# Kernel tuning notes

Hardware: AMD Instinct MI355X
Metric: run time of the kernel (lower is better)

The kernel has to match this reference:

```python
import jax, jax.numpy as jnp
import numpy as np

# Problem sizes: batch B, n variables, m constraints (dense nnz pattern)
B, N, M = 256, 128, 192
# OSQP ADMM parameters (scaling=0, fixed rho; OSQP defaults)
RHO = 0.1      # step size
SIGMA = 1e-6   # regularization
ALPHA = 1.6    # relaxation
N_ITERS = 400  # fixed iteration count (jit-friendly surrogate for max_iter/tolerances)


def setup_inputs() -> dict:
    key = jax.random.key(0)
    k1, k2, k3, k4, k5, k6 = jax.random.split(key, 6)
    G = jax.random.normal(k1, (B, N, N), dtype=jnp.float32)
    # PSD quadratic cost: P = G G^T / n + 0.5 I
    P_val = jnp.einsum('bij,bkj->bik', G, G) / N + 0.5 * jnp.eye(N, dtype=jnp.float32)
    q_val = jax.random.normal(k2, (B, N), dtype=jnp.float32)
    A_val = jax.random.normal(k3, (B, M, N), dtype=jnp.float32) / jnp.sqrt(jnp.float32(N))
    # Bounds bracketing a feasible point x0 so every QP is solvable
    x0 = jax.random.normal(k4, (B, N), dtype=jnp.float32)
    z0 = jnp.einsum('bmn,bn->bm', A_val, x0)
    l_val = z0 - jnp.abs(jax.random.normal(k5, (B, M), dtype=jnp.float32)) - 0.1
    u_val = z0 + jnp.abs(jax.random.normal(k6, (B, M), dtype=jnp.float32)) + 0.1
    return {'P_val': P_val, 'q_val': q_val, 'A_val': A_val,
            'l_val': l_val, 'u_val': u_val}


def _osqp_admm(P, q, A, l, u):
    """Batched OSQP ADMM with fixed rho: solves argmin 1/2 x'Px + q'x s.t. l<=Ax<=u."""
    dt = P.dtype
    I_n = jnp.eye(N, dtype=dt)
    I_m = jnp.eye(M, dtype=dt)
    AT = jnp.swapaxes(A, -1, -2)  # [B, n, m]
    # KKT matrix [[P + sigma*I, A'], [A, -I/rho]]  -> [B, n+m, n+m]
    top = jnp.concatenate([P + SIGMA * I_n, AT], axis=-1)
    bot = jnp.concatenate([A, jnp.broadcast_to(-(1.0 / RHO) * I_m, (P.shape[0], M, M))], axis=-1)
    K = jnp.concatenate([top, bot], axis=-2)
    Kinv = jnp.linalg.inv(K)  # factorize once (rho fixed)

    x0 = jnp.zeros_like(q)
    z0 = jnp.zeros_like(l)
    y0 = jnp.zeros_like(l)

    def step(carry, _):
        x, z, y = carry
        rhs = jnp.concatenate([SIGMA * x - q, z - y / RHO], axis=-1)  # [B, n+m]
        sol = jnp.einsum('bij,bj->bi', Kinv, rhs)
        xt, nu = sol[:, :N], sol[:, N:]
        zt = z + (nu - y) / RHO
        x_new = ALPHA * xt + (1.0 - ALPHA) * x
        zc = ALPHA * zt + (1.0 - ALPHA) * z
        z_new = jnp.clip(zc + y / RHO, l, u)  # projection onto [l, u]
        y_new = y + RHO * (zc - z_new)
        return (x_new, z_new, y_new), None

    (x, z, y), _ = jax.lax.scan(step, (x0, z0, y0), None, length=N_ITERS)
    return x


def reference(P_val, q_val, A_val, l_val, u_val):
    # Returns the batch of primal solutions x_hat, shape [B, n]
    return _osqp_admm(P_val, q_val, A_val, l_val, u_val)
```

## Files before the change

### kernel.cpp

```cpp
#include <hip/hip_runtime.h>


#define Nn 128
#define Mm 192
constexpr float RHO_    = 0.1f;
constexpr float SIGMA_  = 1e-6f;
constexpr float ALPHA_  = 1.6f;
constexpr int   NITERS_ = 400;

typedef float v2f __attribute__((ext_vector_type(2)));
typedef float v4f __attribute__((ext_vector_type(4)));

template<int CTRL>
__device__ __forceinline__ float dpp_add(float x) {
  int y = __builtin_amdgcn_update_dpp(__float_as_int(x), __float_as_int(x),
                                      CTRL, 0xF, 0xF, false);
  return x + __int_as_float(y);
}

template<int K0>
__device__ __forceinline__ void gj_block(float rr[32], float* __restrict__ buf0,
                                         float* __restrict__ buf1,
                                         const int irow, const int qq) {
  const bool qsel = (qq == K0);
  #pragma unroll
  for (int kk = 0; kk < 32; kk++) {
    const int k = 32*K0 + kk;
    float* wb = ((kk & 1) == 0) ? buf0 : buf1;
    if (irow == k) {
      #pragma unroll
      for (int j4 = 0; j4 < 8; j4++)
        *(float4*)&wb[36*qq + 4*j4] = *(const float4*)&rr[4*j4];
    }
    __syncthreads();
    const float akk  = wb[36*K0 + kk];
    float pinv = __builtin_amdgcn_rcpf(akk);
    pinv = pinv + pinv*(1.0f - akk*pinv);
    constexpr int QP = K0 | (K0<<2) | (K0<<4) | (K0<<6);
    const int fi = __builtin_amdgcn_update_dpp(__float_as_int(rr[kk]),
                      __float_as_int(rr[kk]), QP, 0xF, 0xF, false);
    const float f = __int_as_float(fi);
    const bool piv = (irow == k);
    float gfac = f * pinv;
    gfac = piv ? (1.0f - pinv) : gfac;
    float rk[32];
    #pragma unroll
    for (int j4 = 0; j4 < 8; j4++)
      *(float4*)&rk[4*j4] = *(const float4*)&wb[36*qq + 4*j4];
    #pragma unroll
    for (int j = 0; j < 32; j++) rr[j] -= gfac * rk[j];
    const float pivfix = piv ? pinv : -gfac;
    if (qsel) rr[kk] = pivfix;
  }
}

__global__ void __launch_bounds__(512, 2)
precompute_kernel(const float* __restrict__ Pg, const float* __restrict__ qg,
                  const float* __restrict__ Ag, float* __restrict__ wsWt,
                  float* __restrict__ wsC)
{
  __shared__ float smem[16384];
  const int t = threadIdx.x;
  const int b = blockIdx.x;
  const float* __restrict__ Pb = Pg + (size_t)b*Nn*Nn;
  const float* __restrict__ qb = qg + (size_t)b*Nn;
  const float* __restrict__ Ab = Ag + (size_t)b*Mm*Nn;

  {
    const int ar = t & 31;
    const int bc = t >> 5;
    float acc[4][8];
    #pragma unroll
    for (int a=0;a<4;a++)
      #pragma unroll
      for (int j=0;j<8;j++) acc[a][j]=0.f;

    for (int c=0;c<6;c++) {
      __syncthreads();
      {
        const float4* src = (const float4*)(Ab + c*32*Nn);
        float4* dst = (float4*)smem;
        dst[t]     = src[t];
        dst[t+512] = src[t+512];
      }
      __syncthreads();
      #pragma unroll 2
      for (int m=0;m<32;m++) {
        const float4 ra  = *(const float4*)&smem[m*Nn + 4*ar];
        const float4 cb0 = *(const float4*)&smem[m*Nn + 8*bc];
        const float4 cb1 = *(const float4*)&smem[m*Nn + 8*bc + 4];
        const float rv[4] = {ra.x, ra.y, ra.z, ra.w};
        const float cv[8] = {cb0.x,cb0.y,cb0.z,cb0.w,cb1.x,cb1.y,cb1.z,cb1.w};
        #pragma unroll
        for (int a=0;a<4;a++)
          #pragma unroll
          for (int j=0;j<8;j++) acc[a][j] += rv[a]*cv[j];
      }
    }
    __syncthreads();
    #pragma unroll
    for (int a=0;a<4;a++) {
      const int i = 4*ar + a;
      #pragma unroll
      for (int j=0;j<8;j++) {
        const int jj = 8*bc + j;
        float v = Pb[i*Nn + jj] + RHO_*acc[a][j];
        if (i == jj) v += SIGMA_;
        smem[i*Nn + jj] = v;
      }
    }
    __syncthreads();
  }

  {
    const int irow = t >> 2;
    const int qq   = t & 3;
    float rr[32];
    #pragma unroll
    for (int j=0;j<32;j++) rr[j] = smem[irow*Nn + 32*qq + j];
    __syncthreads();
    float* buf0 = smem;
    float* buf1 = smem + 144;
    gj_block<0>(rr, buf0, buf1, irow, qq);
    gj_block<1>(rr, buf0, buf1, irow, qq);
    gj_block<2>(rr, buf0, buf1, irow, qq);
    gj_block<3>(rr, buf0, buf1, irow, qq);
    __syncthreads();
    #pragma unroll
    for (int j=0;j<32;j++) smem[irow*Nn + 32*qq + j] = rr[j];
  }
  __syncthreads();

  {
    const int jr = t & 63, kc = t >> 6;
    v2f acc[3][8];
    #pragma unroll
    for (int a=0;a<3;a++)
      #pragma unroll
      for (int p=0;p<8;p++) acc[a][p] = (v2f){0.f,0.f};

    for (int mi=0; mi<32; mi++) {
      const v4f a0 = *(const v4f*)&Ab[(jr      )*Nn + 4*mi];
      const v4f a1 = *(const v4f*)&Ab[(jr +  64)*Nn + 4*mi];
      const v4f a2 = *(const v4f*)&Ab[(jr + 128)*Nn + 4*mi];
      const float am[3][4] = {{a0.x,a0.y,a0.z,a0.w},
                              {a1.x,a1.y,a1.z,a1.w},
                              {a2.x,a2.y,a2.z,a2.w}};
      #pragma unroll
      for (int q=0;q<4;q++) {
        const int m = 4*mi + q;
        const v4f w0 = *(const v4f*)&smem[m*Nn + 16*kc +  0];
        const v4f w1 = *(const v4f*)&smem[m*Nn + 16*kc +  4];
        const v4f w2 = *(const v4f*)&smem[m*Nn + 16*kc +  8];
        const v4f w3 = *(const v4f*)&smem[m*Nn + 16*kc + 12];
        const v2f wp[8] = {(v2f){w0.x,w0.y},(v2f){w0.z,w0.w},
                           (v2f){w1.x,w1.y},(v2f){w1.z,w1.w},
                           (v2f){w2.x,w2.y},(v2f){w2.z,w2.w},
                           (v2f){w3.x,w3.y},(v2f){w3.z,w3.w}};
        #pragma unroll
        for (int a=0;a<3;a++) {
          const v2f amv = (v2f){am[a][q], am[a][q]};
          #pragma unroll
          for (int p=0;p<8;p++) acc[a][p] += amv * wp[p];
        }
      }
    }
    float* wb = wsWt + (size_t)b*Nn*Mm;
    #pragma unroll
    for (int a=0;a<3;a++) {
      const int j = jr + 64*a;
      #pragma unroll
      for (int p=0;p<8;p++) {
        const int col = 16*kc + 2*p;
        wb[(size_t)(col    )*Mm + j] = acc[a][p].x;
        wb[(size_t)(col + 1)*Mm + j] = acc[a][p].y;
      }
    }
  }
  if (t < Nn) {
    float cc = 0.f;
    #pragma unroll 4
    for (int k=0;k<Nn;k++) cc += smem[k*Nn + t] * qb[k];
    wsC[(size_t)b*Nn + t] = cc;
  }
}

#define WT_LD 196
#define S_SLOT 36
#define S_BUF  (8*S_SLOT)
#define OFF_S0   (Nn*WT_LD)
#define OFF_S1   (OFF_S0 + S_BUF)
#define OFF_SACC (OFF_S1 + S_BUF)
#define OFF_C    (OFF_SACC + Mm)
#define OFF_FLAG (OFF_C + Nn)
#define LOOP_LDS_FLOATS (OFF_FLAG + 2)

__global__ __launch_bounds__(512, 2) void
loop_kernel(const float* __restrict__ Ag, const float* __restrict__ lg,
            const float* __restrict__ ug, const float* __restrict__ wsWtT,
            const float* __restrict__ wsC, float* __restrict__ outg)
{
  extern __shared__ float smem[];
  const int t = threadIdx.x, b = blockIdx.x;
  const int e  = (t & 3) | ((t >> 1) & 4);
  const int rw = ((t >> 2) & 1) | ((t >> 3) & 6);
  const int j0 = ((t >> 6) << 3) | rw;
  const float* __restrict__ Wg = wsWtT + (size_t)b*Nn*Mm;
  const float* __restrict__ cb = wsC  + (size_t)b*Nn;
  const float* __restrict__ Ab = Ag   + (size_t)b*Mm*Nn;

  float* WT    = smem;
  float* sT0   = smem + OFF_S0;
  float* sT1   = smem + OFF_S1;
  float* sacc  = smem + OFF_SACC;
  float* c_s   = smem + OFF_C;
  float* sflag = smem + OFF_FLAG;

  for (int kb = 0; kb < 16; kb++) {
    const int k  = (kb << 3) | (t >> 6);
    const int jc = t & 63;
    WT[k*WT_LD + jc]       = Wg[(size_t)k*Mm + jc];
    WT[k*WT_LD + 64 + jc]  = Wg[(size_t)k*Mm + 64 + jc];
    WT[k*WT_LD + 128 + jc] = Wg[(size_t)k*Mm + 128 + jc];
  }
  if (t < Nn) c_s[t] = cb[t];
  if (t < S_BUF) sT0[t] = 0.f;
  if (t < 2) sflag[t] = 0.f;
  __syncthreads();

  const float* A0 = Ab + (size_t)j0*Nn;
  const float* A1 = A0 + (size_t)64*Nn;
  const float* A2 = A0 + (size_t)128*Nn;
  float lreg[3], ureg[3];
  lreg[0] = lg[(size_t)b*Mm + j0];       ureg[0] = ug[(size_t)b*Mm + j0];
  lreg[1] = lg[(size_t)b*Mm + j0 + 64];  ureg[1] = ug[(size_t)b*Mm + j0 + 64];
  lreg[2] = lg[(size_t)b*Mm + j0 + 128]; ureg[2] = ug[(size_t)b*Mm + j0 + 128];

  float dr[3];
  {
    const float4* cr = (const float4*)(c_s + 16*e);
    const float4 c0 = cr[0], c1 = cr[1], c2 = cr[2], c3 = cr[3];
    const float* Aj[3] = {A0, A1, A2};
    #pragma unroll
    for (int a = 0; a < 3; a++) {
      const float4* ar = (const float4*)(Aj[a] + 16*e);
      const float4 a0 = ar[0], a1 = ar[1], a2 = ar[2], a3 = ar[3];
      float dp = a0.x*c0.x + a0.y*c0.y + a0.z*c0.z + a0.w*c0.w
               + a1.x*c1.x + a1.y*c1.y + a1.z*c1.z + a1.w*c1.w
               + a2.x*c2.x + a2.y*c2.y + a2.z*c2.z + a2.w*c2.w
               + a3.x*c3.x + a3.y*c3.y + a3.z*c3.z + a3.w*c3.w;
      dp = dpp_add<0xB1>(dp);
      dp = dpp_add<0x4E>(dp);
      dp = dpp_add<0x128>(dp);
      dr[a] = dp;
    }
  }

  v2f Ve[3][12];
  #pragma unroll
  for (int a = 0; a < 3; a++)
    #pragma unroll
    for (int p = 0; p < 12; p++) Ve[a][p] = (v2f){0.f, 0.f};
  for (int k4 = 0; k4 < 32; k4++) {
    const v4f a4_0 = *(const v4f*)&A0[4*k4];
    const v4f a4_1 = *(const v4f*)&A1[4*k4];
    const v4f a4_2 = *(const v4f*)&A2[4*k4];
    #pragma unroll
    for (int kk = 0; kk < 4; kk++) {
      const float* wp = &WT[(4*k4 + kk)*WT_LD + 24*e];
      const v4f w0 = *(const v4f*)&wp[0];
      const v4f w1 = *(const v4f*)&wp[4];
      const v4f w2 = *(const v4f*)&wp[8];
      const v4f w3 = *(const v4f*)&wp[12];
      const v4f w4 = *(const v4f*)&wp[16];
      const v4f w5 = *(const v4f*)&wp[20];
      const v2f wv[12] = {(v2f){w0.x,w0.y},(v2f){w0.z,w0.w},
                          (v2f){w1.x,w1.y},(v2f){w1.z,w1.w},
                          (v2f){w2.x,w2.y},(v2f){w2.z,w2.w},
                          (v2f){w3.x,w3.y},(v2f){w3.z,w3.w},
                          (v2f){w4.x,w4.y},(v2f){w4.z,w4.w},
                          (v2f){w5.x,w5.y},(v2f){w5.z,w5.w}};
      const float ax0 = a4_0[kk], ax1 = a4_1[kk], ax2 = a4_2[kk];
      const v2f av0 = (v2f){ax0, ax0};
      const v2f av1 = (v2f){ax1, ax1};
      const v2f av2 = (v2f){ax2, ax2};
      #pragma unroll
      for (int p = 0; p < 12; p++) {
        Ve[0][p] = __builtin_elementwise_fma(av0, wv[p], Ve[0][p]);
        Ve[1][p] = __builtin_elementwise_fma(av1, wv[p], Ve[1][p]);
        Ve[2][p] = __builtin_elementwise_fma(av2, wv[p], Ve[2][p]);
      }
    }
  }

  float sreg[3] = {0.f, 0.f, 0.f};
  float preg[3] = {0.f, 0.f, 0.f};
  float Sacc[3] = {0.f, 0.f, 0.f};
  bool cvg = false;
  const int jsel = j0 + 64*e;
  const int wsel = S_SLOT*(jsel/24) + (jsel%24);
  const bool wr_act = (e < 3);
  const float* rbase0 = sT0 + S_SLOT*e;
  const float* rbase1 = sT1 + S_SLOT*e;

#define ITER(RP, WR, CHK, PH)                                                  \
  {                                                                            \
    const v4f s0 = *(const v4f*)&(RP)[0];                                      \
    const v4f s1 = *(const v4f*)&(RP)[4];                                      \
    const v4f s2 = *(const v4f*)&(RP)[8];                                      \
    const v4f s3 = *(const v4f*)&(RP)[12];                                     \
    const v4f s4 = *(const v4f*)&(RP)[16];                                     \
    const v4f s5 = *(const v4f*)&(RP)[20];                                     \
    const v2f sv[12] = {(v2f){s0.x,s0.y},(v2f){s0.z,s0.w},                     \
                        (v2f){s1.x,s1.y},(v2f){s1.z,s1.w},                     \
                        (v2f){s2.x,s2.y},(v2f){s2.z,s2.w},                     \
                        (v2f){s3.x,s3.y},(v2f){s3.z,s3.w},                     \
                        (v2f){s4.x,s4.y},(v2f){s4.z,s4.w},                     \
                        (v2f){s5.x,s5.y},(v2f){s5.z,s5.w}};                    \
    v2f x0[3], x1[3];                                                          \
    _Pragma("unroll")                                                          \
    for (int a = 0; a < 3; a++) { x0[a]=(v2f){0.f,0.f}; x1[a]=(v2f){0.f,0.f}; }\
    _Pragma("unroll")                                                          \
    for (int p = 0; p < 6; p++) {                                              \
      _Pragma("unroll")                                                        \
      for (int a = 0; a < 3; a++) {                                            \
        x0[a] = __builtin_elementwise_fma(Ve[a][2*p],   sv[2*p],   x0[a]);     \
        x1[a] = __builtin_elementwise_fma(Ve[a][2*p+1], sv[2*p+1], x1[a]);     \
      }                                                                        \
    }                                                                          \
    float sn[3], pn[3];                                                        \
    _Pragma("unroll")                                                          \
    for (int a = 0; a < 3; a++) {                                              \
      const v2f xs = x0[a] + x1[a];                                            \
      float pr = xs.x + xs.y;                                                  \
      pr = dpp_add<0xB1>(pr);                                                  \
      pr = dpp_add<0x4E>(pr);                                                  \
      pr = dpp_add<0x128>(pr);                                                 \
      const float w_ = pr - dr[a];                                             \
      const float v_ = fmaf(ALPHA_, w_, preg[a]);                              \
      const float z_ = __builtin_amdgcn_fmed3f(v_, lreg[a], ureg[a]);          \
      sn[a] = RHO_ * fmaf(2.0f, z_, -v_);                                      \
      pn[a] = fmaf(-ALPHA_, z_, v_);                                           \
    }                                                                          \
    const float vsel = (e == 1) ? sn[1] : ((e == 2) ? sn[2] : sn[0]);          \
    if (wr_act) (WR)[wsel] = vsel;                                             \
    if (CHK) {                                                                 \
      if (!(sn[0]==sreg[0] && pn[0]==preg[0] &&                                \
            sn[1]==sreg[1] && pn[1]==preg[1] &&                                \
            sn[2]==sreg[2] && pn[2]==preg[2])) sflag[PH] = 1.f;                \
    }                                                                          \
    _Pragma("unroll")                                                          \
    for (int a = 0; a < 3; a++) {                                              \
      Sacc[a] = fmaf(1.0f - ALPHA_, Sacc[a], ALPHA_ * sreg[a]);                \
      sreg[a] = sn[a]; preg[a] = pn[a];                                        \
    }                                                                          \
    if ((CHK) && t == 0) sflag[(PH) ^ 1] = 0.f;                                \
    __syncthreads();                                                           \
    if (CHK) cvg = (sflag[PH] == 0.f);                                         \
  }

  #pragma unroll 1
  for (int it2 = 0; it2 < NITERS_/2; it2++) {
    ITER(rbase0, sT1, false, 0)
    const bool chk = ((it2 & 3) == 3) && (it2 < NITERS_/2 - 40);
    const int ph = (it2 >> 2) & 1;
    ITER(rbase1, sT0, chk, ph)
    if (cvg) break;
  }
#undef ITER
  if (cvg) {
    #pragma unroll
    for (int a = 0; a < 3; a++) Sacc[a] = sreg[a];
  }

  if (wr_act) {
    const float ssel = (e == 1) ? Sacc[1] : ((e == 2) ? Sacc[2] : Sacc[0]);
    sacc[jsel] = ssel;
  }
  __syncthreads();
  if (t < Nn) {
    const float* wr = &WT[t*WT_LD];
    v2f xa = (v2f){0.f,0.f}, xb = (v2f){0.f,0.f};
    #pragma unroll
    for (int j4 = 0; j4 < 48; j4++) {
      const v4f wv = *(const v4f*)&wr[4*j4];
      const v4f sv = *(const v4f*)&sacc[4*j4];
      xa = __builtin_elementwise_fma((v2f){wv.x,wv.y}, (v2f){sv.x,sv.y}, xa);
      xb = __builtin_elementwise_fma((v2f){wv.z,wv.w}, (v2f){sv.z,sv.w}, xb);
    }
    xa += xb;
    outg[(size_t)b*Nn + t] = xa.x + xa.y - c_s[t];
  }
}

extern "C" void kernel_launch(void* const* d_in, const int* in_sizes, int n_in,
                              void* d_out, int out_size, void* d_ws, size_t ws_size,
                              hipStream_t stream) {
  const float* P = (const float*)d_in[0];
  const float* q = (const float*)d_in[1];
  const float* A = (const float*)d_in[2];
  const float* l = (const float*)d_in[3];
  const float* u = (const float*)d_in[4];
  (void)in_sizes; (void)n_in; (void)out_size; (void)ws_size;
  float* wsWt = (float*)d_ws;
  float* wsC  = wsWt + (size_t)256*Mm*Nn;
  precompute_kernel<<<256, 512, 0, stream>>>(P, q, A, wsWt, wsC);
  loop_kernel<<<256, 512, LOOP_LDS_FLOATS*4, stream>>>(A, l, u, wsWt, wsC, (float*)d_out);
}
```

Baseline: 404.1 us.

## Double loop-kernel threads to 1024 and split each row's reduction across 16 lanes

The ADMM loop kernel now runs 1024 threads per block instead of 512. Each constraint row's dot product is spread over 16 lanes instead of 8, so every lane holds half as many register-resident matrix entries and the per-iteration FMA chain is shorter. The cross-lane reduction becomes a 16-lane DPP row reduction, and the W staging load is vectorised with float4. The cost is an extra reduction step per iteration and more waves contending at each __syncthreads barrier.

```diff
diff --git a/kernel.cpp b/kernel.cpp
--- a/kernel.cpp
+++ b/kernel.cpp
@@ -16,6 +16,11 @@
   int y = __builtin_amdgcn_update_dpp(__float_as_int(x), __float_as_int(x),
                                       CTRL, 0xF, 0xF, false);
   return x + __int_as_float(y);
+}
+__device__ __forceinline__ float red16(float x) {
+  x = dpp_add<0x121>(x); x = dpp_add<0x122>(x);
+  x = dpp_add<0x124>(x); x = dpp_add<0x128>(x);
+  return x;
 }
 
 template<int K0>
@@ -195,16 +200,15 @@
 #define OFF_FLAG (OFF_C + Nn)
 #define LOOP_LDS_FLOATS (OFF_FLAG + 2)
 
-__global__ __launch_bounds__(512, 2) void
+__global__ __launch_bounds__(1024, 4) void
 loop_kernel(const float* __restrict__ Ag, const float* __restrict__ lg,
             const float* __restrict__ ug, const float* __restrict__ wsWtT,
             const float* __restrict__ wsC, float* __restrict__ outg)
 {
   extern __shared__ float smem[];
   const int t = threadIdx.x, b = blockIdx.x;
-  const int e  = (t & 3) | ((t >> 1) & 4);
-  const int rw = ((t >> 2) & 1) | ((t >> 3) & 6);
-  const int j0 = ((t >> 6) << 3) | rw;
+  const int f  = t & 15;
+  const int j0 = t >> 4;
   const float* __restrict__ Wg = wsWtT + (size_t)b*Nn*Mm;
   const float* __restrict__ cb = wsC  + (size_t)b*Nn;
   const float* __restrict__ Ab = Ag   + (size_t)b*Mm*Nn;
@@ -216,12 +220,13 @@
   float* c_s   = smem + OFF_C;
   float* sflag = smem + OFF_FLAG;
 
-  for (int kb = 0; kb < 16; kb++) {
-    const int k  = (kb << 3) | (t >> 6);
-    const int jc = t & 63;
-    WT[k*WT_LD + jc]       = Wg[(size_t)k*Mm + jc];
-    WT[k*WT_LD + 64 + jc]  = Wg[(size_t)k*Mm + 64 + jc];
-    WT[k*WT_LD + 128 + jc] = Wg[(size_t)k*Mm + 128 + jc];
+  {
+    const int k  = t >> 3;
+    const int cbase = (t & 7) * 24;
+    #pragma unroll
+    for (int i = 0; i < 6; i++)
+      *(float4*)&WT[k*WT_LD + cbase + 4*i] =
+        *(const float4*)&Wg[(size_t)k*Mm + cbase + 4*i];
   }
   if (t < Nn) c_s[t] = cb[t];
   if (t < S_BUF) sT0[t] = 0.f;
@@ -238,54 +243,43 @@
 
   float dr[3];
   {
-    const float4* cr = (const float4*)(c_s + 16*e);
-    const float4 c0 = cr[0], c1 = cr[1], c2 = cr[2], c3 = cr[3];
+    const float4* cr = (const float4*)(c_s + 8*f);
+    const float4 c0 = cr[0], c1 = cr[1];
     const float* Aj[3] = {A0, A1, A2};
     #pragma unroll
     for (int a = 0; a < 3; a++) {
-      const float4* ar = (const float4*)(Aj[a] + 16*e);
-      const float4 a0 = ar[0], a1 = ar[1], a2 = ar[2], a3 = ar[3];
+      const float4* ar = (const float4*)(Aj[a] + 8*f);
+      const float4 a0 = ar[0], a1 = ar[1];
       float dp = a0.x*c0.x + a0.y*c0.y + a0.z*c0.z + a0.w*c0.w
-               + a1.x*c1.x + a1.y*c1.y + a1.z*c1.z + a1.w*c1.w
-               + a2.x*c2.x + a2.y*c2.y + a2.z*c2.z + a2.w*c2.w
-               + a3.x*c3.x + a3.y*c3.y + a3.z*c3.z + a3.w*c3.w;
-      dp = dpp_add<0xB1>(dp);
-      dp = dpp_add<0x4E>(dp);
-      dp = dpp_add<0x128>(dp);
-      dr[a] = dp;
-    }
-  }
-
-  v2f Ve[3][12];
+               + a1.x*c1.x + a1.y*c1.y + a1.z*c1.z + a1.w*c1.w;
+      dr[a] = red16(dp);
+    }
+  }
+
+  v2f Ve[3][6];
   #pragma unroll
   for (int a = 0; a < 3; a++)
     #pragma unroll
-    for (int p = 0; p < 12; p++) Ve[a][p] = (v2f){0.f, 0.f};
+    for (int p = 0; p < 6; p++) Ve[a][p] = (v2f){0.f, 0.f};
   for (int k4 = 0; k4 < 32; k4++) {
     const v4f a4_0 = *(const v4f*)&A0[4*k4];
     const v4f a4_1 = *(const v4f*)&A1[4*k4];
     const v4f a4_2 = *(const v4f*)&A2[4*k4];
     #pragma unroll
     for (int kk = 0; kk < 4; kk++) {
-      const float* wp = &WT[(4*k4 + kk)*WT_LD + 24*e];
+      const float* wp = &WT[(4*k4 + kk)*WT_LD + 12*f];
       const v4f w0 = *(const v4f*)&wp[0];
       const v4f w1 = *(const v4f*)&wp[4];
       const v4f w2 = *(const v4f*)&wp[8];
-      const v4f w3 = *(const v4f*)&wp[12];
-      const v4f w4 = *(const v4f*)&wp[16];
-      const v4f w5 = *(const v4f*)&wp[20];
-      const v2f wv[12] = {(v2f){w0.x,w0.y},(v2f){w0.z,w0.w},
-                          (v2f){w1.x,w1.y},(v2f){w1.z,w1.w},
-                          (v2f){w2.x,w2.y},(v2f){w2.z,w2.w},
-                          (v2f){w3.x,w3.y},(v2f){w3.z,w3.w},
-                          (v2f){w4.x,w4.y},(v2f){w4.z,w4.w},
-                          (v2f){w5.x,w5.y},(v2f){w5.z,w5.w}};
+      const v2f wv[6] = {(v2f){w0.x,w0.y},(v2f){w0.z,w0.w},
+                         (v2f){w1.x,w1.y},(v2f){w1.z,w1.w},
+                         (v2f){w2.x,w2.y},(v2f){w2.z,w2.w}};
       const float ax0 = a4_0[kk], ax1 = a4_1[kk], ax2 = a4_2[kk];
       const v2f av0 = (v2f){ax0, ax0};
       const v2f av1 = (v2f){ax1, ax1};
       const v2f av2 = (v2f){ax2, ax2};
       #pragma unroll
-      for (int p = 0; p < 12; p++) {
+      for (int p = 0; p < 6; p++) {
         Ve[0][p] = __builtin_elementwise_fma(av0, wv[p], Ve[0][p]);
         Ve[1][p] = __builtin_elementwise_fma(av1, wv[p], Ve[1][p]);
         Ve[2][p] = __builtin_elementwise_fma(av2, wv[p], Ve[2][p]);
@@ -297,55 +291,44 @@
   float preg[3] = {0.f, 0.f, 0.f};
   float Sacc[3] = {0.f, 0.f, 0.f};
   bool cvg = false;
-  const int jsel = j0 + 64*e;
-  const int wsel = S_SLOT*(jsel/24) + (jsel%24);
-  const bool wr_act = (e < 3);
-  const float* rbase0 = sT0 + S_SLOT*e;
-  const float* rbase1 = sT1 + S_SLOT*e;
+  const int fs   = (f < 3) ? f : 0;
+  const int jw   = j0 + 64*fs;
+  const int wsel = S_SLOT*(jw/24) + (jw%24);
+  const bool wr_act = (f < 3);
+  const float* rbase0 = sT0 + S_SLOT*(f >> 1) + 12*(f & 1);
+  const float* rbase1 = sT1 + S_SLOT*(f >> 1) + 12*(f & 1);
 
 #define ITER(RP, WR, CHK, PH)                                                  \
   {                                                                            \
     const v4f s0 = *(const v4f*)&(RP)[0];                                      \
     const v4f s1 = *(const v4f*)&(RP)[4];                                      \
     const v4f s2 = *(const v4f*)&(RP)[8];                                      \
-    const v4f s3 = *(const v4f*)&(RP)[12];                                     \
-    const v4f s4 = *(const v4f*)&(RP)[16];                                     \
-    const v4f s5 = *(const v4f*)&(RP)[20];                                     \
-    const v2f sv[12] = {(v2f){s0.x,s0.y},(v2f){s0.z,s0.w},                     \
-                        (v2f){s1.x,s1.y},(v2f){s1.z,s1.w},                     \
-                        (v2f){s2.x,s2.y},(v2f){s2.z,s2.w},                     \
-                        (v2f){s3.x,s3.y},(v2f){s3.z,s3.w},                     \
-                        (v2f){s4.x,s4.y},(v2f){s4.z,s4.w},                     \
-                        (v2f){s5.x,s5.y},(v2f){s5.z,s5.w}};                    \
-    v2f x0[3], x1[3];                                                          \
-    _Pragma("unroll")                                                          \
-    for (int a = 0; a < 3; a++) { x0[a]=(v2f){0.f,0.f}; x1[a]=(v2f){0.f,0.f}; }\
-    _Pragma("unroll")                                                          \
-    for (int p = 0; p < 6; p++) {                                              \
-      _Pragma("unroll")                                                        \
-      for (int a = 0; a < 3; a++) {                                            \
-        x0[a] = __builtin_elementwise_fma(Ve[a][2*p],   sv[2*p],   x0[a]);     \
-        x1[a] = __builtin_elementwise_fma(Ve[a][2*p+1], sv[2*p+1], x1[a]);     \
-      }                                                                        \
-    }                                                                          \
+    const v2f sva = (v2f){s0.x,s0.y}, svb = (v2f){s0.z,s0.w};                  \
+    const v2f svc = (v2f){s1.x,s1.y}, svd = (v2f){s1.z,s1.w};                  \
+    const v2f sve = (v2f){s2.x,s2.y}, svf = (v2f){s2.z,s2.w};                  \
     float sn[3], pn[3];                                                        \
     _Pragma("unroll")                                                          \
     for (int a = 0; a < 3; a++) {                                              \
-      const v2f xs = x0[a] + x1[a];                                            \
-      float pr = xs.x + xs.y;                                                  \
-      pr = dpp_add<0xB1>(pr);                                                  \
-      pr = dpp_add<0x4E>(pr);                                                  \
-      pr = dpp_add<0x128>(pr);                                                 \
+      v2f x0 = (v2f){0.f,0.f}, x1 = (v2f){0.f,0.f};                            \
+      x0 = __builtin_elementwise_fma(Ve[a][0], sva, x0);                       \
+      x1 = __builtin_elementwise_fma(Ve[a][1], svb, x1);                       \
+      x0 = __builtin_elementwise_fma(Ve[a][2], svc, x0);                       \
+      x1 = __builtin_elementwise_fma(Ve[a][3], svd, x1);                       \
+      x0 = __builtin_elementwise_fma(Ve[a][4], sve, x0);                       \
+      x1 = __builtin_elementwise_fma(Ve[a][5], svf, x1);                       \
+      const v2f xs = x0 + x1;                                                  \
+      const float pr = red16(xs.x + xs.y);                                     \
       const float w_ = pr - dr[a];                                             \
       const float v_ = fmaf(ALPHA_, w_, preg[a]);                              \
       const float z_ = __builtin_amdgcn_fmed3f(v_, lreg[a], ureg[a]);          \
       sn[a] = RHO_ * fmaf(2.0f, z_, -v_);                                      \
       pn[a] = fmaf(-ALPHA_, z_, v_);                                           \
     }                                                                          \
-    const float vsel = (e == 1) ? sn[1] : ((e == 2) ? sn[2] : sn[0]);          \
+    const float vsel = (f == 1) ? sn[1] : ((f == 2) ? sn[2] : sn[0]);          \
     if (wr_act) (WR)[wsel] = vsel;                                             \
     if (CHK) {                                                                 \
-      if (!(sn[0]==sreg[0] && pn[0]==preg[0] &&                                \
+      if (f == 0 &&                                                            \
+          !(sn[0]==sreg[0] && pn[0]==preg[0] &&                                \
             sn[1]==sreg[1] && pn[1]==preg[1] &&                                \
             sn[2]==sreg[2] && pn[2]==preg[2])) sflag[PH] = 1.f;                \
     }                                                                          \
@@ -374,8 +357,8 @@
   }
 
   if (wr_act) {
-    const float ssel = (e == 1) ? Sacc[1] : ((e == 2) ? Sacc[2] : Sacc[0]);
-    sacc[jsel] = ssel;
+    const float ssel = (f == 1) ? Sacc[1] : ((f == 2) ? Sacc[2] : Sacc[0]);
+    sacc[jw] = ssel;
   }
   __syncthreads();
   if (t < Nn) {
@@ -405,5 +388,5 @@
   float* wsWt = (float*)d_ws;
   float* wsC  = wsWt + (size_t)256*Mm*Nn;
   precompute_kernel<<<256, 512, 0, stream>>>(P, q, A, wsWt, wsC);
-  loop_kernel<<<256, 512, LOOP_LDS_FLOATS*4, stream>>>(A, l, u, wsWt, wsC, (float*)d_out);
-}
+  loop_kernel<<<256, 1024, LOOP_LDS_FLOATS*4, stream>>>(A, l, u, wsWt, wsC, (float*)d_out);
+}
```

Result: slower. 504.8 us (+24.9%).

## Fuse precompute and ADMM loop kernels, keeping W and c in LDS

Applied to the files above, without the earlier changes.

Merges the precompute kernel (matrix inverse and W = A·Pinv product) into the iteration kernel. W and c are written straight into shared memory instead of round-tripping through a global workspace, which removes one launch and the global write and reload of W. It also reorders the per-iteration dot product into four independent accumulator chains and clamps jsel so lanes with e>=3 index safely. In exchange, the fused kernel needs dynamic LDS sized for the loop layout (about 100KB) while the precompute phase reuses that region. This could affect occupancy, and the serial phases now share one block.

```diff
diff --git a/kernel.cpp b/kernel.cpp
--- a/kernel.cpp
+++ b/kernel.cpp
@@ -17,6 +17,16 @@
                                       CTRL, 0xF, 0xF, false);
   return x + __int_as_float(y);
 }
+
+#define WT_LD 196
+#define S_SLOT 36
+#define S_BUF  (8*S_SLOT)
+#define OFF_S0   (Nn*WT_LD)
+#define OFF_S1   (OFF_S0 + S_BUF)
+#define OFF_SACC (OFF_S1 + S_BUF)
+#define OFF_C    (OFF_SACC + Mm)
+#define OFF_FLAG (OFF_C + Nn)
+#define FUSED_LDS_FLOATS (OFF_FLAG + 2)
 
 template<int K0>
 __device__ __forceinline__ void gj_block(float rr[32], float* __restrict__ buf0,
@@ -54,17 +64,24 @@
   }
 }
 
-__global__ void __launch_bounds__(512, 2)
-precompute_kernel(const float* __restrict__ Pg, const float* __restrict__ qg,
-                  const float* __restrict__ Ag, float* __restrict__ wsWt,
-                  float* __restrict__ wsC)
+__global__ __launch_bounds__(512, 2) void
+fused_kernel(const float* __restrict__ Pg, const float* __restrict__ qg,
+             const float* __restrict__ Ag, const float* __restrict__ lg,
+             const float* __restrict__ ug, float* __restrict__ outg)
 {
-  __shared__ float smem[16384];
+  extern __shared__ float smem[];
   const int t = threadIdx.x;
   const int b = blockIdx.x;
   const float* __restrict__ Pb = Pg + (size_t)b*Nn*Nn;
   const float* __restrict__ qb = qg + (size_t)b*Nn;
   const float* __restrict__ Ab = Ag + (size_t)b*Mm*Nn;
+
+  float* WT    = smem;
+  float* sT0   = smem + OFF_S0;
+  float* sT1   = smem + OFF_S1;
+  float* sacc  = smem + OFF_SACC;
+  float* c_s   = smem + OFF_C;
+  float* sflag = smem + OFF_FLAG;
 
   {
     const int ar = t & 31;
@@ -130,6 +147,13 @@
     for (int j=0;j<32;j++) smem[irow*Nn + 32*qq + j] = rr[j];
   }
   __syncthreads();
+
+  if (t < Nn) {
+    float cc = 0.f;
+    #pragma unroll 4
+    for (int k=0;k<Nn;k++) cc += smem[k*Nn + t] * qb[k];
+    c_s[t] = cc;
+  }
 
   {
     const int jr = t & 63, kc = t >> 6;
@@ -165,68 +189,25 @@
         }
       }
     }
-    float* wb = wsWt + (size_t)b*Nn*Mm;
+    __syncthreads();
     #pragma unroll
     for (int a=0;a<3;a++) {
       const int j = jr + 64*a;
       #pragma unroll
       for (int p=0;p<8;p++) {
         const int col = 16*kc + 2*p;
-        wb[(size_t)(col    )*Mm + j] = acc[a][p].x;
-        wb[(size_t)(col + 1)*Mm + j] = acc[a][p].y;
-      }
-    }
-  }
-  if (t < Nn) {
-    float cc = 0.f;
-    #pragma unroll 4
-    for (int k=0;k<Nn;k++) cc += smem[k*Nn + t] * qb[k];
-    wsC[(size_t)b*Nn + t] = cc;
-  }
-}
-
-#define WT_LD 196
-#define S_SLOT 36
-#define S_BUF  (8*S_SLOT)
-#define OFF_S0   (Nn*WT_LD)
-#define OFF_S1   (OFF_S0 + S_BUF)
-#define OFF_SACC (OFF_S1 + S_BUF)
-#define OFF_C    (OFF_SACC + Mm)
-#define OFF_FLAG (OFF_C + Nn)
-#define LOOP_LDS_FLOATS (OFF_FLAG + 2)
-
-__global__ __launch_bounds__(512, 2) void
-loop_kernel(const float* __restrict__ Ag, const float* __restrict__ lg,
-            const float* __restrict__ ug, const float* __restrict__ wsWtT,
-            const float* __restrict__ wsC, float* __restrict__ outg)
-{
-  extern __shared__ float smem[];
-  const int t = threadIdx.x, b = blockIdx.x;
+        WT[(col    )*WT_LD + j] = acc[a][p].x;
+        WT[(col + 1)*WT_LD + j] = acc[a][p].y;
+      }
+    }
+  }
+  if (t < S_BUF) sT0[t] = 0.f;
+  if (t < 2) sflag[t] = 0.f;
+  __syncthreads();
+
   const int e  = (t & 3) | ((t >> 1) & 4);
   const int rw = ((t >> 2) & 1) | ((t >> 3) & 6);
   const int j0 = ((t >> 6) << 3) | rw;
-  const float* __restrict__ Wg = wsWtT + (size_t)b*Nn*Mm;
-  const float* __restrict__ cb = wsC  + (size_t)b*Nn;
-  const float* __restrict__ Ab = Ag   + (size_t)b*Mm*Nn;
-
-  float* WT    = smem;
-  float* sT0   = smem + OFF_S0;
-  float* sT1   = smem + OFF_S1;
-  float* sacc  = smem + OFF_SACC;
-  float* c_s   = smem + OFF_C;
-  float* sflag = smem + OFF_FLAG;
-
-  for (int kb = 0; kb < 16; kb++) {
-    const int k  = (kb << 3) | (t >> 6);
-    const int jc = t & 63;
-    WT[k*WT_LD + jc]       = Wg[(size_t)k*Mm + jc];
-    WT[k*WT_LD + 64 + jc]  = Wg[(size_t)k*Mm + 64 + jc];
-    WT[k*WT_LD + 128 + jc] = Wg[(size_t)k*Mm + 128 + jc];
-  }
-  if (t < Nn) c_s[t] = cb[t];
-  if (t < S_BUF) sT0[t] = 0.f;
-  if (t < 2) sflag[t] = 0.f;
-  __syncthreads();
 
   const float* A0 = Ab + (size_t)j0*Nn;
   const float* A1 = A0 + (size_t)64*Nn;
@@ -297,7 +278,7 @@
   float preg[3] = {0.f, 0.f, 0.f};
   float Sacc[3] = {0.f, 0.f, 0.f};
   bool cvg = false;
-  const int jsel = j0 + 64*e;
+  const int jsel = j0 + 64*((e < 3) ? e : 0);
   const int wsel = S_SLOT*(jsel/24) + (jsel%24);
   const bool wr_act = (e < 3);
   const float* rbase0 = sT0 + S_SLOT*e;
@@ -317,22 +298,23 @@
                         (v2f){s3.x,s3.y},(v2f){s3.z,s3.w},                     \
                         (v2f){s4.x,s4.y},(v2f){s4.z,s4.w},                     \
                         (v2f){s5.x,s5.y},(v2f){s5.z,s5.w}};                    \
-    v2f x0[3], x1[3];                                                          \
-    _Pragma("unroll")                                                          \
-    for (int a = 0; a < 3; a++) { x0[a]=(v2f){0.f,0.f}; x1[a]=(v2f){0.f,0.f}; }\
-    _Pragma("unroll")                                                          \
-    for (int p = 0; p < 6; p++) {                                              \
-      _Pragma("unroll")                                                        \
-      for (int a = 0; a < 3; a++) {                                            \
-        x0[a] = __builtin_elementwise_fma(Ve[a][2*p],   sv[2*p],   x0[a]);     \
-        x1[a] = __builtin_elementwise_fma(Ve[a][2*p+1], sv[2*p+1], x1[a]);     \
-      }                                                                        \
-    }                                                                          \
     float sn[3], pn[3];                                                        \
     _Pragma("unroll")                                                          \
     for (int a = 0; a < 3; a++) {                                              \
-      const v2f xs = x0[a] + x1[a];                                            \
-      float pr = xs.x + xs.y;                                                  \
+      v2f x0 = Ve[a][0] * sv[0];                                               \
+      v2f x1 = Ve[a][1] * sv[1];                                               \
+      v2f x2 = Ve[a][2] * sv[2];                                               \
+      v2f x3 = Ve[a][3] * sv[3];                                               \
+      x0 = __builtin_elementwise_fma(Ve[a][4], sv[4], x0);                     \
+      x1 = __builtin_elementwise_fma(Ve[a][5], sv[5], x1);                     \
+      x2 = __builtin_elementwise_fma(Ve[a][6], sv[6], x2);                     \
+      x3 = __builtin_elementwise_fma(Ve[a][7], sv[7], x3);                     \
+      x0 = __builtin_elementwise_fma(Ve[a][8], sv[8], x0);                     \
+      x1 = __builtin_elementwise_fma(Ve[a][9], sv[9], x1);                     \
+      x2 = __builtin_elementwise_fma(Ve[a][10], sv[10], x2);                   \
+      x3 = __builtin_elementwise_fma(Ve[a][11], sv[11], x3);                   \
+      x0 += x1; x2 += x3; x0 += x2;                                            \
+      float pr = x0.x + x0.y;                                                  \
       pr = dpp_add<0xB1>(pr);                                                  \
       pr = dpp_add<0x4E>(pr);                                                  \
       pr = dpp_add<0x128>(pr);                                                 \
@@ -401,9 +383,6 @@
   const float* A = (const float*)d_in[2];
   const float* l = (const float*)d_in[3];
   const float* u = (const float*)d_in[4];
-  (void)in_sizes; (void)n_in; (void)out_size; (void)ws_size;
-  float* wsWt = (float*)d_ws;
-  float* wsC  = wsWt + (size_t)256*Mm*Nn;
-  precompute_kernel<<<256, 512, 0, stream>>>(P, q, A, wsWt, wsC);
-  loop_kernel<<<256, 512, LOOP_LDS_FLOATS*4, stream>>>(A, l, u, wsWt, wsC, (float*)d_out);
+  (void)in_sizes; (void)n_in; (void)out_size; (void)d_ws; (void)ws_size;
+  fused_kernel<<<256, 512, FUSED_LDS_FLOATS*4, stream>>>(P, q, A, l, u, (float*)d_out);
 }
```

New measurement: 429.9 us. +6.4%, slower.
